# Performance work log

Hardware: AMD Instinct MI355X
Metric: run time of the kernel (lower is better)

The kernel has to match this reference:

```python
import jax, jax.numpy as jnp
import numpy as np

N_NODES = 50000
N_EDGES = 500000
D_NODE = 256
D_EDGE = 256
FINAL_OUT = 256
NEG_SLOPE = 0.01  # torch LeakyReLU default


def _linear_params(key, d_in, d_out):
    kw, kb = jax.random.split(key)
    s = 1.0 / np.sqrt(d_in)
    W = jax.random.uniform(kw, (d_in, d_out), jnp.float32, -s, s)
    b = jax.random.uniform(kb, (d_out,), jnp.float32, -s, s)
    return W, b


def setup_inputs() -> dict:
    key = jax.random.key(0)
    ks = jax.random.split(key, 8)
    in1 = D_NODE + D_EDGE          # 512
    hid1 = 2 * in1                 # 1024
    out1 = hid1 // 2               # 512
    in2 = out1 + D_NODE            # 768
    hid2 = 2 * in2                 # 1536
    W1, b1 = _linear_params(ks[0], in1, hid1)
    W2, b2 = _linear_params(ks[1], hid1, out1)
    W3, b3 = _linear_params(ks[2], in2, hid2)
    W4, b4 = _linear_params(ks[3], hid2, FINAL_OUT)
    x = jax.random.normal(ks[4], (N_NODES, D_NODE), jnp.float32)
    edge_attr = jax.random.normal(ks[5], (N_EDGES, D_EDGE), jnp.float32)
    edge_index = jax.random.randint(ks[6], (2, N_EDGES), 0, N_NODES, jnp.int64)
    u = jax.random.normal(ks[7], (1, 16), jnp.float32)
    batch = jnp.zeros((N_NODES,), jnp.int64)
    return {"x": x, "edge_index": edge_index, "edge_attr": edge_attr,
            "u": u, "batch": batch,
            "W1": W1, "b1": b1, "W2": W2, "b2": b2,
            "W3": W3, "b3": b3, "W4": W4, "b4": b4}


def _leaky(v):
    return jnp.where(v >= 0, v, NEG_SLOPE * v)


def reference(x, edge_index, edge_attr, u, batch, W1, b1, W2, b2, W3, b3, W4, b4):
    row, col = edge_index[0], edge_index[1]
    # gather source-node features and concat edge features: [E, D_NODE+D_EDGE]
    m = jnp.concatenate([x[row], edge_attr], axis=1)
    # node_mlp_1
    m = _leaky(m @ W1 + b1) @ W2 + b2            # [E, out1]
    # scatter-mean over destination nodes (count clamped to 1, as torch_scatter)
    agg = jax.ops.segment_sum(m, col, num_segments=x.shape[0])
    cnt = jax.ops.segment_sum(jnp.ones((m.shape[0],), m.dtype), col,
                              num_segments=x.shape[0])
    agg = agg / jnp.maximum(cnt, 1.0)[:, None]   # [N, out1]
    # node_mlp_2
    h = jnp.concatenate([x, agg], axis=1)        # [N, in2]
    return _leaky(h @ W3 + b3) @ W4 + b4         # [N, FINAL_OUT]
```

## Files before the change

### kernel.cpp

```cpp
#include <hip/hip_runtime.h>

typedef __bf16 bf16x8 __attribute__((ext_vector_type(8)));
typedef float fx4 __attribute__((ext_vector_type(4)));
typedef unsigned short u16x8 __attribute__((ext_vector_type(8)));
typedef unsigned short u16x4 __attribute__((ext_vector_type(4)));

__device__ __forceinline__ unsigned short f2b(float f) {
  unsigned u = __float_as_uint(f);
  u = (u + 0x7fffu + ((u >> 16) & 1u)) >> 16;
  return (unsigned short)u;
}

__device__ __forceinline__ void gload16(const void* g, void* l) {
  __builtin_amdgcn_global_load_lds(
      (const __attribute__((address_space(1))) unsigned int*)g,
      (__attribute__((address_space(3))) unsigned int*)l, 16, 0, 0);
}

template<int MODE, int K, int N, int NT, bool EAB>
__global__ __launch_bounds__(256)
void gemm_k(const unsigned short* __restrict__ A,
            const unsigned short* __restrict__ xb,
            const unsigned short* __restrict__ eab,
            const float* __restrict__ eaf,
            const float* __restrict__ aggH_in,
            const float* __restrict__ cnt,
            const unsigned short* __restrict__ agg2b_in,
            const int* __restrict__ perm,
            const int* __restrict__ ssrc,
            const int* __restrict__ sdst,
            const unsigned short* __restrict__ Bt,
            const float* __restrict__ bias,
            float* __restrict__ outf,
            unsigned short* __restrict__ outb,
            int M, int base, int mt, int mtc)
{
  const int bid = blockIdx.x;
  const int xcd = bid & 7;
  const int sl  = bid >> 3;
  const int tile_n = sl % NT;
  const int tile_m = xcd * mtc + sl / NT;
  if (tile_m >= mt) return;

  __shared__ __align__(16) char smem[18688];
  unsigned short* Al = (unsigned short*)smem;
  unsigned short* Bl = (unsigned short*)(smem + 8192);

  const int t = threadIdx.x;
  const int w = t >> 6, l = t & 63;
  const int wr = w >> 1, wc = w & 1;
  const int lr = l & 15, lk = l >> 4;

  fx4 zero = {0.f, 0.f, 0.f, 0.f};
  fx4 acc[4][4];
#pragma unroll
  for (int i = 0; i < 4; i++)
#pragma unroll
    for (int j = 0; j < 4; j++) acc[i][j] = zero;

  for (int k0 = 0; k0 < K; k0 += 32) {
#pragma unroll
    for (int it = 0; it < 2; ++it) {
      const int c = t + it * 256;
      const int row = c >> 2, u = c & 3;
      gload16(Bt + (size_t)(tile_n * 128 + row) * K + (k0 + u * 8),
              (char*)Bl + c * 16);
      int rl = tile_m * 128 + row; if (rl >= M) rl = M - 1;
      if constexpr (MODE == 1) {
        if (k0 < 256) {
          const int node = ssrc[rl];
          gload16(xb + (size_t)node * 256 + (k0 + u * 8), (char*)Al + c * 16);
        } else {
          const int e = perm[rl];
          if constexpr (EAB) {
            gload16(eab + (size_t)e * 256 + (k0 - 256) + u * 8,
                    (char*)Al + c * 16);
          } else {
            const float* s = eaf + (size_t)e * 256 + (k0 - 256) + u * 8;
            fx4 f0 = *(const fx4*)s, f1 = *(const fx4*)(s + 4);
            u16x8 v;
            v[0]=f2b(f0[0]); v[1]=f2b(f0[1]); v[2]=f2b(f0[2]); v[3]=f2b(f0[3]);
            v[4]=f2b(f1[0]); v[5]=f2b(f1[1]); v[6]=f2b(f1[2]); v[7]=f2b(f1[3]);
            *(u16x8*)((char*)Al + c * 16) = v;
          }
        }
      } else if constexpr (MODE == 2) {
        const float ct = cnt[rl];
        const float rs = 1.f / fmaxf(ct, 1.f);
        const float* s = aggH_in + (size_t)rl * 1024 + (k0 + u * 8);
        fx4 f0 = *(const fx4*)s, f1 = *(const fx4*)(s + 4);
        u16x8 v;
        v[0]=f2b(f0[0]*rs); v[1]=f2b(f0[1]*rs); v[2]=f2b(f0[2]*rs); v[3]=f2b(f0[3]*rs);
        v[4]=f2b(f1[0]*rs); v[5]=f2b(f1[1]*rs); v[6]=f2b(f1[2]*rs); v[7]=f2b(f1[3]*rs);
        *(u16x8*)((char*)Al + c * 16) = v;
      } else if constexpr (MODE == 3) {
        const int node = base + rl;
        if (k0 < 256)
          gload16(xb + (size_t)node * 256 + (k0 + u * 8), (char*)Al + c * 16);
        else
          gload16(agg2b_in + (size_t)node * 512 + (k0 - 256) + u * 8,
                  (char*)Al + c * 16);
      } else {
        gload16(A + (size_t)rl * K + (k0 + u * 8), (char*)Al + c * 16);
      }
    }
    __syncthreads();

    bf16x8 af[4], bfr[4];
    const int mb0 = wr * 64, nb0 = wc * 64;
#pragma unroll
    for (int i = 0; i < 4; i++)
      af[i] = *(const bf16x8*)(Al + (mb0 + i * 16 + lr) * 32 + lk * 8);
#pragma unroll
    for (int j = 0; j < 4; j++)
      bfr[j] = *(const bf16x8*)(Bl + (nb0 + j * 16 + lr) * 32 + lk * 8);
#pragma unroll
    for (int i = 0; i < 4; i++)
#pragma unroll
      for (int j = 0; j < 4; j++)
        acc[i][j] = __builtin_amdgcn_mfma_f32_16x16x32_bf16(af[i], bfr[j],
                                                            acc[i][j], 0, 0, 0);
    __syncthreads();
  }

  if constexpr (MODE == 1) {
    const int mbase = tile_m * 128;
    int rows = M - mbase; if (rows > 128) rows = 128;
    float* CL = (float*)smem;
    int* runs_s = (int*)(smem + 16896);
    int* runs_e = (int*)(smem + 17408);
    int* runs_d = (int*)(smem + 17920);
    unsigned long long* wmask = (unsigned long long*)(smem + 18432);
    int flag = 0;
    if (t < 128)
      flag = (t < rows) && ((t == 0) || (sdst[mbase + t] != sdst[mbase + t - 1]));
    unsigned long long bm = __ballot(flag);
    if (l == 0 && w < 2) wmask[w] = bm;
    __syncthreads();
    const unsigned long long m0 = wmask[0], m1 = wmask[1];
    const int nruns = __builtin_popcountll(m0) + __builtin_popcountll(m1);
    if (flag) {
      int rank, rend;
      if (t < 64) {
        rank = __builtin_popcountll(m0 & ((t == 0) ? 0ull : ((1ull << t) - 1)));
        unsigned long long above = (t == 63) ? 0ull : (m0 & (~0ull << (t + 1)));
        if (above) rend = __builtin_ctzll(above);
        else if (m1) rend = 64 + __builtin_ctzll(m1);
        else rend = rows;
      } else {
        const int tt = t - 64;
        rank = __builtin_popcountll(m0) +
               __builtin_popcountll(m1 & ((tt == 0) ? 0ull : ((1ull << tt) - 1)));
        unsigned long long above = (tt == 63) ? 0ull : (m1 & (~0ull << (tt + 1)));
        rend = above ? 64 + __builtin_ctzll(above) : rows;
      }
      runs_s[rank] = t; runs_e[rank] = rend; runs_d[rank] = sdst[mbase + t];
    }
    const int lc = wc * 16 + lr;
    const int nn_base = tile_n * 128 + wc * 64 + lr;
#pragma unroll
    for (int j = 0; j < 4; ++j) {
      const float bj = bias[nn_base + j * 16];
#pragma unroll
      for (int i = 0; i < 4; i++)
#pragma unroll
        for (int r = 0; r < 4; r++) {
          float v = acc[i][j][r] + bj;
          v = v >= 0.f ? v : 0.01f * v;
          CL[(wr * 64 + i * 16 + lk * 4 + r) * 33 + lc] = v;
        }
      __syncthreads();
      for (int task = t; task < nruns * 32; task += 256) {
        const int ri = task >> 5, c = task & 31;
        const int rs = runs_s[ri], re = runs_e[ri];
        float s = 0.f;
        for (int r = rs; r < re; ++r) s += CL[r * 33 + c];
        const int n = tile_n * 128 + (c >> 4) * 64 + j * 16 + (c & 15);
        float* addr = outf + (size_t)runs_d[ri] * 1024 + n;
        const bool open = (rs == 0 && mbase > 0) || (re == rows && mbase + rows < M);
        if (open) atomicAdd(addr, s); else *addr = s;
      }
      __syncthreads();
    }
  } else {
#pragma unroll
    for (int j = 0; j < 4; j++) {
      const int n = tile_n * 128 + wc * 64 + j * 16 + lr;
      const float bj = bias[n];
#pragma unroll
      for (int i = 0; i < 4; i++) {
        const int m0 = tile_m * 128 + wr * 64 + i * 16 + lk * 4;
#pragma unroll
        for (int r = 0; r < 4; r++) {
          const int m = m0 + r;
          if (m < M) {
            float v = acc[i][j][r];
            if constexpr (MODE == 2) {
              v += (cnt[m] > 0.f ? bj : 0.f);
              outb[(size_t)m * N + n] = f2b(v);
            } else if constexpr (MODE == 3) {
              v += bj;
              v = v >= 0.f ? v : 0.01f * v;
              outb[(size_t)m * N + n] = f2b(v);
            } else {
              outf[(size_t)(base + m) * N + n] = v + bj;
            }
          }
        }
      }
    }
  }
}

__global__ void fix_idx_k(const int* __restrict__ src, int* __restrict__ dst, int n2) {
  int i = blockIdx.x * blockDim.x + threadIdx.x;
  if (i >= n2) return;
  bool is64 = true;
#pragma unroll
  for (int p = 0; p < 16; ++p) is64 = is64 && (src[2 * p + 1] == 0);
  dst[i] = is64 ? src[2 * i] : src[i];
}

__global__ void cvt_f2b_k(const float* __restrict__ x, unsigned short* __restrict__ o,
                          long n4) {
  long i = (long)blockIdx.x * blockDim.x + threadIdx.x;
  if (i < n4) {
    fx4 f = *(const fx4*)(x + i * 4);
    u16x4 v; v[0]=f2b(f[0]); v[1]=f2b(f[1]); v[2]=f2b(f[2]); v[3]=f2b(f[3]);
    *(u16x4*)(o + i * 4) = v;
  }
}

__global__ void cvt_w_k(const float* __restrict__ W, unsigned short* __restrict__ Wt,
                        int K, int N) {
  long i = (long)blockIdx.x * blockDim.x + threadIdx.x;
  if (i < (long)K * N) {
    int k = (int)(i / N), n = (int)(i % N);
    Wt[(size_t)n * K + k] = f2b(W[i]);
  }
}

__global__ void cnt_kk(const int* __restrict__ ecol, float* __restrict__ cnt, int E) {
  int i = blockIdx.x * blockDim.x + threadIdx.x;
  if (i < E) atomicAdd(cnt + ecol[i], 1.f);
}

__global__ __launch_bounds__(1024)
void scan_k(const float* __restrict__ cnt, int* __restrict__ pos, int Nn) {
  __shared__ int sdata[1024];
  __shared__ int carry;
  if (threadIdx.x == 0) carry = 0;
  __syncthreads();
  for (int bb = 0; bb < Nn; bb += 1024) {
    const int i = bb + threadIdx.x;
    const int v = (i < Nn) ? (int)cnt[i] : 0;
    sdata[threadIdx.x] = v;
    __syncthreads();
    for (int off = 1; off < 1024; off <<= 1) {
      int tv = (threadIdx.x >= off) ? sdata[threadIdx.x - off] : 0;
      __syncthreads();
      sdata[threadIdx.x] += tv;
      __syncthreads();
    }
    const int excl = sdata[threadIdx.x] - v + carry;
    if (i < Nn) pos[i] = excl;
    __syncthreads();
    if (threadIdx.x == 1023) carry += sdata[1023];
    __syncthreads();
  }
}

__global__ void perm_k(const int* __restrict__ idx, int E, int* __restrict__ pos,
                       int* __restrict__ perm, int* __restrict__ ssrc,
                       int* __restrict__ sdst) {
  int e = blockIdx.x * blockDim.x + threadIdx.x;
  if (e >= E) return;
  const int d = idx[E + e];
  const int s = atomicAdd(pos + d, 1);
  perm[s] = e;
  ssrc[s] = idx[e];
  sdst[s] = d;
}

extern "C" void kernel_launch(void* const* d_in, const int* in_sizes, int n_in,
                              void* d_out, int out_size, void* d_ws, size_t ws_size,
                              hipStream_t stream)
{
  const float* x  = (const float*)d_in[0];
  const int* eraw = (const int*)d_in[1];
  const float* ea = (const float*)d_in[2];
  const float* W1 = (const float*)d_in[5];
  const float* b1 = (const float*)d_in[6];
  const float* W2 = (const float*)d_in[7];
  const float* b2 = (const float*)d_in[8];
  const float* W3 = (const float*)d_in[9];
  const float* b3 = (const float*)d_in[10];
  const float* W4 = (const float*)d_in[11];
  const float* b4 = (const float*)d_in[12];
  float* out = (float*)d_out;

  const int Nn = in_sizes[0] / 256;
  const int E  = in_sizes[1] / 2;

  char* p = (char*)d_ws;
  auto take = [&](size_t bytes) -> char* {
    char* r = p; p += (bytes + 255) & ~(size_t)255; return r;
  };
  unsigned short* W1t = (unsigned short*)take((size_t)512 * 1024 * 2);
  unsigned short* W2t = (unsigned short*)take((size_t)1024 * 512 * 2);
  unsigned short* W3t = (unsigned short*)take((size_t)768 * 1536 * 2);
  unsigned short* W4t = (unsigned short*)take((size_t)1536 * 256 * 2);
  int* idx  = (int*)take((size_t)2 * E * 4);
  float* cnt  = (float*)take((size_t)Nn * 4);
  float* aggH = (float*)take((size_t)Nn * 1024 * 4);
  size_t zlen = (size_t)(p - (char*)cnt);
  unsigned short* agg2b = (unsigned short*)take((size_t)Nn * 512 * 2);
  unsigned short* xb    = (unsigned short*)take((size_t)Nn * 256 * 2);
  int* pos  = (int*)take((size_t)Nn * 4);
  int* perm = (int*)take((size_t)E * 4);
  int* ssrc = (int*)take((size_t)E * 4);
  int* sdst = (int*)take((size_t)E * 4);

  long avail = (long)ws_size - (long)(p - (char*)d_ws);

  unsigned short* eab = nullptr;
  const long eab_bytes = (((long)E * 256 * 2) + 255) & ~255L;
  if (avail >= eab_bytes + 128 * 3072 + 1024) {
    eab = (unsigned short*)take((size_t)E * 256 * 2);
    avail -= eab_bytes;
  }
  long bandN = avail / 3072;  bandN &= ~127L;
  if (bandN > 50048) bandN = 50048;
  if (bandN < 128)   bandN = 128;
  unsigned short* H3 = (unsigned short*)take((size_t)bandN * 3072);

  hipMemsetAsync(cnt, 0, zlen, stream);
  fix_idx_k<<<(2 * E + 255) / 256, 256, 0, stream>>>(eraw, idx, 2 * E);
  cnt_kk<<<(E + 255) / 256, 256, 0, stream>>>(idx + E, cnt, E);
  scan_k<<<1, 1024, 0, stream>>>(cnt, pos, Nn);
  perm_k<<<(E + 255) / 256, 256, 0, stream>>>(idx, E, pos, perm, ssrc, sdst);
  cvt_f2b_k<<<(Nn * 64 + 255) / 256, 256, 0, stream>>>(x, xb, (long)Nn * 64);
  if (eab)
    cvt_f2b_k<<<(int)(((long)E * 64 + 255) / 256), 256, 0, stream>>>(ea, eab,
                                                                     (long)E * 64);
  cvt_w_k<<<(512 * 1024 + 255) / 256, 256, 0, stream>>>(W1, W1t, 512, 1024);
  cvt_w_k<<<(1024 * 512 + 255) / 256, 256, 0, stream>>>(W2, W2t, 1024, 512);
  cvt_w_k<<<(768 * 1536 + 255) / 256, 256, 0, stream>>>(W3, W3t, 768, 1536);
  cvt_w_k<<<(1536 * 256 + 255) / 256, 256, 0, stream>>>(W4, W4t, 1536, 256);

  {
    const int mt = (E + 127) / 128, mtc = (mt + 7) / 8;
    const int grid = mtc * 8 * 8;
    if (eab)
      gemm_k<1, 512, 1024, 8, true><<<grid, 256, 0, stream>>>(
          nullptr, xb, eab, ea, nullptr, nullptr, nullptr, perm, ssrc, sdst,
          W1t, b1, aggH, nullptr, E, 0, mt, mtc);
    else
      gemm_k<1, 512, 1024, 8, false><<<grid, 256, 0, stream>>>(
          nullptr, xb, nullptr, ea, nullptr, nullptr, nullptr, perm, ssrc, sdst,
          W1t, b1, aggH, nullptr, E, 0, mt, mtc);
  }

  {
    const int mt = (Nn + 127) / 128, mtc = (mt + 7) / 8;
    gemm_k<2, 1024, 512, 4, false><<<mtc * 8 * 4, 256, 0, stream>>>(
        nullptr, nullptr, nullptr, nullptr, aggH, cnt, nullptr, nullptr,
        nullptr, nullptr, W2t, b2, nullptr, agg2b, Nn, 0, mt, mtc);
  }

  for (long base = 0; base < Nn; base += bandN) {
    long rem = Nn - base;
    int mb = (int)(rem < bandN ? rem : bandN);
    int mt = (mb + 127) / 128, mtc = (mt + 7) / 8;
    gemm_k<3, 768, 1536, 12, false><<<mtc * 8 * 12, 256, 0, stream>>>(
        nullptr, xb, nullptr, nullptr, nullptr, nullptr, agg2b, nullptr,
        nullptr, nullptr, W3t, b3, nullptr, H3, mb, (int)base, mt, mtc);
    gemm_k<4, 1536, 256, 2, false><<<mtc * 8 * 2, 256, 0, stream>>>(
        H3, nullptr, nullptr, nullptr, nullptr, nullptr, nullptr, nullptr,
        nullptr, nullptr, W4t, b4, out, nullptr, mb, (int)base, mt, mtc);
  }
}
```

Before: 1.784 ms.

## Precompute per-node x@W1 projection and pre-sort edge attributes by destination

Splits the first edge MLP layer so the x[row]@W1_top part runs once per node (a 50k-row GEMM into a bf16 table) rather than once per edge. The edge GEMM now has K=256 and adds the gathered per-node projection in its epilogue. Edge attributes are also converted to bf16 already permuted into sorted order, so the edge GEMM loads them contiguously. This halves the largest GEMM's FLOPs but adds a gather of 1024-wide bf16 rows per edge in the epilogue, an extra intermediate rounding to bf16, and a 100MB scratch table.

After: 2.630 ms. 47.4% more time.

```diff
diff --git a/kernel.cpp b/kernel.cpp
--- a/kernel.cpp
+++ b/kernel.cpp
@@ -10,6 +10,9 @@
   u = (u + 0x7fffu + ((u >> 16) & 1u)) >> 16;
   return (unsigned short)u;
 }
+__device__ __forceinline__ float b2f(unsigned short s) {
+  return __uint_as_float((unsigned)s << 16);
+}
 
 __device__ __forceinline__ void gload16(const void* g, void* l) {
   __builtin_amdgcn_global_load_lds(
@@ -21,11 +24,12 @@
 __global__ __launch_bounds__(256)
 void gemm_k(const unsigned short* __restrict__ A,
             const unsigned short* __restrict__ xb,
-            const unsigned short* __restrict__ eab,
+            const unsigned short* __restrict__ eas,
             const float* __restrict__ eaf,
             const float* __restrict__ aggH_in,
             const float* __restrict__ cnt,
             const unsigned short* __restrict__ agg2b_in,
+            const unsigned short* __restrict__ zxb,
             const int* __restrict__ perm,
             const int* __restrict__ ssrc,
             const int* __restrict__ sdst,
@@ -67,22 +71,16 @@
               (char*)Bl + c * 16);
       int rl = tile_m * 128 + row; if (rl >= M) rl = M - 1;
       if constexpr (MODE == 1) {
-        if (k0 < 256) {
-          const int node = ssrc[rl];
-          gload16(xb + (size_t)node * 256 + (k0 + u * 8), (char*)Al + c * 16);
+        if constexpr (EAB) {
+          gload16(eas + (size_t)rl * 256 + (k0 + u * 8), (char*)Al + c * 16);
         } else {
           const int e = perm[rl];
-          if constexpr (EAB) {
-            gload16(eab + (size_t)e * 256 + (k0 - 256) + u * 8,
-                    (char*)Al + c * 16);
-          } else {
-            const float* s = eaf + (size_t)e * 256 + (k0 - 256) + u * 8;
-            fx4 f0 = *(const fx4*)s, f1 = *(const fx4*)(s + 4);
-            u16x8 v;
-            v[0]=f2b(f0[0]); v[1]=f2b(f0[1]); v[2]=f2b(f0[2]); v[3]=f2b(f0[3]);
-            v[4]=f2b(f1[0]); v[5]=f2b(f1[1]); v[6]=f2b(f1[2]); v[7]=f2b(f1[3]);
-            *(u16x8*)((char*)Al + c * 16) = v;
-          }
+          const float* s = eaf + (size_t)e * 256 + (k0 + u * 8);
+          fx4 f0 = *(const fx4*)s, f1 = *(const fx4*)(s + 4);
+          u16x8 v;
+          v[0]=f2b(f0[0]); v[1]=f2b(f0[1]); v[2]=f2b(f0[2]); v[3]=f2b(f0[3]);
+          v[4]=f2b(f1[0]); v[5]=f2b(f1[1]); v[6]=f2b(f1[2]); v[7]=f2b(f1[3]);
+          *(u16x8*)((char*)Al + c * 16) = v;
         }
       } else if constexpr (MODE == 2) {
         const float ct = cnt[rl];
@@ -100,6 +98,8 @@
         else
           gload16(agg2b_in + (size_t)node * 512 + (k0 - 256) + u * 8,
                   (char*)Al + c * 16);
+      } else if constexpr (MODE == 5) {
+        gload16(xb + (size_t)rl * 256 + (k0 + u * 8), (char*)Al + c * 16);
       } else {
         gload16(A + (size_t)rl * K + (k0 + u * 8), (char*)Al + c * 16);
       }
@@ -156,16 +156,27 @@
       }
       runs_s[rank] = t; runs_e[rank] = rend; runs_d[rank] = sdst[mbase + t];
     }
+    int sn[16];
+#pragma unroll
+    for (int i = 0; i < 4; i++)
+#pragma unroll
+      for (int r = 0; r < 4; r++) {
+        const int g = mbase + wr * 64 + i * 16 + lk * 4 + r;
+        sn[i * 4 + r] = (g < M) ? ssrc[g] : -1;
+      }
     const int lc = wc * 16 + lr;
     const int nn_base = tile_n * 128 + wc * 64 + lr;
 #pragma unroll
     for (int j = 0; j < 4; ++j) {
-      const float bj = bias[nn_base + j * 16];
+      const int ncol = nn_base + j * 16;
+      const float bj = bias[ncol];
 #pragma unroll
       for (int i = 0; i < 4; i++)
 #pragma unroll
         for (int r = 0; r < 4; r++) {
+          const int s = sn[i * 4 + r];
           float v = acc[i][j][r] + bj;
+          if (s >= 0) v += b2f(zxb[(size_t)s * 1024 + ncol]);
           v = v >= 0.f ? v : 0.01f * v;
           CL[(wr * 64 + i * 16 + lk * 4 + r) * 33 + lc] = v;
         }
@@ -186,7 +197,8 @@
 #pragma unroll
     for (int j = 0; j < 4; j++) {
       const int n = tile_n * 128 + wc * 64 + j * 16 + lr;
-      const float bj = bias[n];
+      float bj = 0.f;
+      if constexpr (MODE != 5) bj = bias[n];
 #pragma unroll
       for (int i = 0; i < 4; i++) {
         const int m0 = tile_m * 128 + wr * 64 + i * 16 + lk * 4;
@@ -202,6 +214,8 @@
               v += bj;
               v = v >= 0.f ? v : 0.01f * v;
               outb[(size_t)m * N + n] = f2b(v);
+            } else if constexpr (MODE == 5) {
+              outb[(size_t)m * N + n] = f2b(v);
             } else {
               outf[(size_t)(base + m) * N + n] = v + bj;
             }
@@ -229,6 +243,17 @@
     u16x4 v; v[0]=f2b(f[0]); v[1]=f2b(f[1]); v[2]=f2b(f[2]); v[3]=f2b(f[3]);
     *(u16x4*)(o + i * 4) = v;
   }
+}
+
+__global__ void cvt_eas_k(const float* __restrict__ ea, const int* __restrict__ perm,
+                          unsigned short* __restrict__ eas, int E) {
+  long i = (long)blockIdx.x * blockDim.x + threadIdx.x;
+  if (i >= (long)E * 64) return;
+  const int s = (int)(i >> 6), q = (int)(i & 63);
+  const float* src = ea + (size_t)perm[s] * 256 + q * 4;
+  fx4 f = *(const fx4*)src;
+  u16x4 v; v[0]=f2b(f[0]); v[1]=f2b(f[1]); v[2]=f2b(f[2]); v[3]=f2b(f[3]);
+  *(u16x4*)(eas + (size_t)s * 256 + q * 4) = v;
 }
 
 __global__ void cvt_w_k(const float* __restrict__ W, unsigned short* __restrict__ Wt,
@@ -306,16 +331,18 @@
   auto take = [&](size_t bytes) -> char* {
     char* r = p; p += (bytes + 255) & ~(size_t)255; return r;
   };
-  unsigned short* W1t = (unsigned short*)take((size_t)512 * 1024 * 2);
-  unsigned short* W2t = (unsigned short*)take((size_t)1024 * 512 * 2);
-  unsigned short* W3t = (unsigned short*)take((size_t)768 * 1536 * 2);
-  unsigned short* W4t = (unsigned short*)take((size_t)1536 * 256 * 2);
+  unsigned short* W1xt = (unsigned short*)take((size_t)1024 * 256 * 2);
+  unsigned short* W1et = (unsigned short*)take((size_t)1024 * 256 * 2);
+  unsigned short* W2t  = (unsigned short*)take((size_t)1024 * 512 * 2);
+  unsigned short* W3t  = (unsigned short*)take((size_t)768 * 1536 * 2);
+  unsigned short* W4t  = (unsigned short*)take((size_t)1536 * 256 * 2);
   int* idx  = (int*)take((size_t)2 * E * 4);
   float* cnt  = (float*)take((size_t)Nn * 4);
   float* aggH = (float*)take((size_t)Nn * 1024 * 4);
   size_t zlen = (size_t)(p - (char*)cnt);
   unsigned short* agg2b = (unsigned short*)take((size_t)Nn * 512 * 2);
   unsigned short* xb    = (unsigned short*)take((size_t)Nn * 256 * 2);
+  unsigned short* zxb   = (unsigned short*)take((size_t)Nn * 1024 * 2);
   int* pos  = (int*)take((size_t)Nn * 4);
   int* perm = (int*)take((size_t)E * 4);
   int* ssrc = (int*)take((size_t)E * 4);
@@ -323,11 +350,11 @@
 
   long avail = (long)ws_size - (long)(p - (char*)d_ws);
 
-  unsigned short* eab = nullptr;
-  const long eab_bytes = (((long)E * 256 * 2) + 255) & ~255L;
-  if (avail >= eab_bytes + 128 * 3072 + 1024) {
-    eab = (unsigned short*)take((size_t)E * 256 * 2);
-    avail -= eab_bytes;
+  unsigned short* eas = nullptr;
+  const long eas_bytes = (((long)E * 256 * 2) + 255) & ~255L;
+  if (avail >= eas_bytes + 128 * 3072 + 1024) {
+    eas = (unsigned short*)take((size_t)E * 256 * 2);
+    avail -= eas_bytes;
   }
   long bandN = avail / 3072;  bandN &= ~127L;
   if (bandN > 50048) bandN = 50048;
@@ -340,32 +367,41 @@
   scan_k<<<1, 1024, 0, stream>>>(cnt, pos, Nn);
   perm_k<<<(E + 255) / 256, 256, 0, stream>>>(idx, E, pos, perm, ssrc, sdst);
   cvt_f2b_k<<<(Nn * 64 + 255) / 256, 256, 0, stream>>>(x, xb, (long)Nn * 64);
-  if (eab)
-    cvt_f2b_k<<<(int)(((long)E * 64 + 255) / 256), 256, 0, stream>>>(ea, eab,
-                                                                     (long)E * 64);
-  cvt_w_k<<<(512 * 1024 + 255) / 256, 256, 0, stream>>>(W1, W1t, 512, 1024);
+  if (eas)
+    cvt_eas_k<<<(int)(((long)E * 64 + 255) / 256), 256, 0, stream>>>(ea, perm,
+                                                                     eas, E);
+  cvt_w_k<<<(256 * 1024 + 255) / 256, 256, 0, stream>>>(W1, W1xt, 256, 1024);
+  cvt_w_k<<<(256 * 1024 + 255) / 256, 256, 0, stream>>>(W1 + 256 * 1024, W1et,
+                                                        256, 1024);
   cvt_w_k<<<(1024 * 512 + 255) / 256, 256, 0, stream>>>(W2, W2t, 1024, 512);
   cvt_w_k<<<(768 * 1536 + 255) / 256, 256, 0, stream>>>(W3, W3t, 768, 1536);
   cvt_w_k<<<(1536 * 256 + 255) / 256, 256, 0, stream>>>(W4, W4t, 1536, 256);
 
   {
+    const int mt = (Nn + 127) / 128, mtc = (mt + 7) / 8;
+    gemm_k<5, 256, 1024, 8, false><<<mtc * 8 * 8, 256, 0, stream>>>(
+        nullptr, xb, nullptr, nullptr, nullptr, nullptr, nullptr, nullptr,
+        nullptr, nullptr, nullptr, W1xt, nullptr, nullptr, zxb, Nn, 0, mt, mtc);
+  }
+
+  {
     const int mt = (E + 127) / 128, mtc = (mt + 7) / 8;
     const int grid = mtc * 8 * 8;
-    if (eab)
-      gemm_k<1, 512, 1024, 8, true><<<grid, 256, 0, stream>>>(
-          nullptr, xb, eab, ea, nullptr, nullptr, nullptr, perm, ssrc, sdst,
-          W1t, b1, aggH, nullptr, E, 0, mt, mtc);
+    if (eas)
+      gemm_k<1, 256, 1024, 8, true><<<grid, 256, 0, stream>>>(
+          nullptr, nullptr, eas, ea, nullptr, nullptr, nullptr, zxb, perm,
+          ssrc, sdst, W1et, b1, aggH, nullptr, E, 0, mt, mtc);
     else
-      gemm_k<1, 512, 1024, 8, false><<<grid, 256, 0, stream>>>(
-          nullptr, xb, nullptr, ea, nullptr, nullptr, nullptr, perm, ssrc, sdst,
-          W1t, b1, aggH, nullptr, E, 0, mt, mtc);
+      gemm_k<1, 256, 1024, 8, false><<<grid, 256, 0, stream>>>(
+          nullptr, nullptr, nullptr, ea, nullptr, nullptr, nullptr, zxb, perm,
+          ssrc, sdst, W1et, b1, aggH, nullptr, E, 0, mt, mtc);
   }
 
   {
     const int mt = (Nn + 127) / 128, mtc = (mt + 7) / 8;
     gemm_k<2, 1024, 512, 4, false><<<mtc * 8 * 4, 256, 0, stream>>>(
         nullptr, nullptr, nullptr, nullptr, aggH, cnt, nullptr, nullptr,
-        nullptr, nullptr, W2t, b2, nullptr, agg2b, Nn, 0, mt, mtc);
+        nullptr, nullptr, nullptr, W2t, b2, nullptr, agg2b, Nn, 0, mt, mtc);
   }
 
   for (long base = 0; base < Nn; base += bandN) {
@@ -374,9 +410,9 @@
     int mt = (mb + 127) / 128, mtc = (mt + 7) / 8;
     gemm_k<3, 768, 1536, 12, false><<<mtc * 8 * 12, 256, 0, stream>>>(
         nullptr, xb, nullptr, nullptr, nullptr, nullptr, agg2b, nullptr,
-        nullptr, nullptr, W3t, b3, nullptr, H3, mb, (int)base, mt, mtc);
+        nullptr, nullptr, nullptr, W3t, b3, nullptr, H3, mb, (int)base, mt, mtc);
     gemm_k<4, 1536, 256, 2, false><<<mtc * 8 * 2, 256, 0, stream>>>(
         H3, nullptr, nullptr, nullptr, nullptr, nullptr, nullptr, nullptr,
-        nullptr, nullptr, W4t, b4, out, nullptr, mb, (int)base, mt, mtc);
-  }
-}
+        nullptr, nullptr, nullptr, W4t, b4, out, nullptr, mb, (int)base, mt, mtc);
+  }
+}
```
